# Optimization experiments

Measured on AMD Instinct MI355X. Metric: run time of the kernel, lower is better.

Reference implementation:

```python
import jax, jax.numpy as jnp
import numpy as np

HEADS = 8
DIM_HEAD = 32
DIM = 256
HIDDEN = HEADS * DIM_HEAD  # 256


def setup_inputs() -> dict:
    key = jax.random.key(0)
    ks = jax.random.split(key, 6)
    B, T, C, H, W = 4, 16, DIM, 32, 32
    x = jax.random.normal(ks[0], (B, T, C, H, W), dtype=jnp.float32)
    rel_pos = jax.random.normal(ks[1], (HEADS, T, T), dtype=jnp.float32)
    # 1x1 conv weights == channel-mixing matrices
    w_qkv = jax.random.normal(ks[2], (3 * HIDDEN, C), dtype=jnp.float32) * (C ** -0.5)
    b_qkv = jnp.zeros((3 * HIDDEN,), dtype=jnp.float32)
    w_out = jax.random.normal(ks[3], (C, HIDDEN), dtype=jnp.float32) * (HIDDEN ** -0.5)
    b_out = jnp.zeros((C,), dtype=jnp.float32)
    return {"x": x, "rel_pos": rel_pos, "w_qkv": w_qkv, "b_qkv": b_qkv,
            "w_out": w_out, "b_out": b_out}


def reference(x, rel_pos, w_qkv, b_qkv, w_out, b_out):
    B, T, C, H, W = x.shape
    scale = DIM_HEAD ** -0.5
    # 1x1 conv QKV projection: (B,T,C,H,W) x (3*hidden, C) -> (B,T,H,W,3*hidden)
    qkv = jnp.einsum('btchw,oc->bthwo', x, w_qkv) + b_qkv
    q, k, v = jnp.split(qkv, 3, axis=-1)
    # split heads: (B,T,H,W,heads,dim_head); attention over T per (b,h,w,head)
    q = q.reshape(B, T, H, W, HEADS, DIM_HEAD) * scale
    k = k.reshape(B, T, H, W, HEADS, DIM_HEAD)
    v = v.reshape(B, T, H, W, HEADS, DIM_HEAD)
    # sim: (B,H,W,heads,T,T)
    sim = jnp.einsum('bihwnd,bjhwnd->bhwnij', q, k)
    sim = sim + rel_pos  # (heads,T,T) broadcasts over (B,H,W)
    attn = jax.nn.softmax(sim, axis=-1)
    out = jnp.einsum('bhwnij,bjhwnd->bihwnd', attn, v)  # (B,T,H,W,heads,dh)
    out = out.reshape(B, T, H, W, HIDDEN)
    # 1x1 conv output projection back to C channels
    y = jnp.einsum('bthwe,ce->bthwc', out, w_out) + b_out
    return jnp.transpose(y, (0, 1, 4, 2, 3))  # (B,T,C,H,W)
```

## Files before the change

kernel.cpp:

```cpp
#include <hip/hip_runtime.h>
#include <hip/hip_bf16.h>

typedef __attribute__((ext_vector_type(8))) short bf16x8;
typedef __attribute__((ext_vector_type(4))) float f32x4;
typedef __attribute__((ext_vector_type(16))) float f32x16;

namespace {

constexpr int kT = 16;
constexpr int kC = 256;
constexpr int kHW = 1024;

__device__ __forceinline__ unsigned short f2bf(float f) {
  unsigned int x;
  __builtin_memcpy(&x, &f, 4);
  x += 0x7fff + ((x >> 16) & 1);
  return (unsigned short)(x >> 16);
}
__device__ __forceinline__ unsigned int pack2(float a, float b) {
  return (unsigned int)f2bf(a) | ((unsigned int)f2bf(b) << 16);
}

__global__ __launch_bounds__(256) void prep(const float* __restrict__ x,
                                            const float* __restrict__ wqkv,
                                            const float* __restrict__ wout,
                                            unsigned short* __restrict__ xT,
                                            unsigned short* __restrict__ wAll) {
  __shared__ unsigned short ts[64 * 72];
  const int bx = blockIdx.x;
  const int tid = threadIdx.x;
  if (bx < 4096) {
    const int cc = bx & 3, hc = (bx >> 2) & 15, t = (bx >> 6) & 15, b = bx >> 10;
    const int c0 = cc * 64, hw0 = hc * 64;
    {
      const int ci = tid >> 2, j = tid & 3;
      const float* xrow = x + (((size_t)(b * 16 + t) * 256 + c0 + ci) * 1024) + hw0;
#pragma unroll
      for (int u = 0; u < 4; ++u) {
        const int chunk = j + u * 4;
        const float4 v = *(const float4*)(xrow + chunk * 4);
        const int hwl = chunk * 4;
        ts[(hwl + 0) * 72 + ci] = f2bf(v.x);
        ts[(hwl + 1) * 72 + ci] = f2bf(v.y);
        ts[(hwl + 2) * 72 + ci] = f2bf(v.z);
        ts[(hwl + 3) * 72 + ci] = f2bf(v.w);
      }
    }
    __syncthreads();
    {
      const int hwp = tid >> 2, jp = tid & 3;
      const uint4 a = *(const uint4*)&ts[hwp * 72 + jp * 16];
      const uint4 bq = *(const uint4*)&ts[hwp * 72 + jp * 16 + 8];
      unsigned short* dst =
          xT + ((size_t)((b * 1024 + hw0 + hwp) * 16 + t) * 256) + c0 + jp * 16;
      *(uint4*)dst = a;
      *(uint4*)(dst + 8) = bq;
    }
  } else {
    const int g = bx - 4096;
    const int row_l = tid >> 3;
    const int seg = tid & 7;
    const float* src;
    int srow;
    if (g < 24) { src = wqkv; srow = (g % 3) * 256 + (g / 3) * 32 + row_l; }
    else        { src = wout; srow = (g - 24) * 32 + row_l; }
    const float* s = src + (size_t)srow * 256 + seg * 32;
    unsigned short* d = wAll + ((size_t)(g * 32 + row_l)) * 256 + seg * 32;
#pragma unroll
    for (int u = 0; u < 8; ++u) {
      const float4 v = *(const float4*)(s + u * 4);
      uint2 p;
      p.x = pack2(v.x, v.y);
      p.y = pack2(v.z, v.w);
      *(uint2*)(d + u * 4) = p;
    }
  }
}

constexpr int kWBStride = 264;
constexpr int kWBTile = 32 * kWBStride;
constexpr int kWB = 2 * kWBTile;
constexpr int kSite = 1824;
constexpr int kSmem = kWB + 8 * kSite;
static_assert(kSmem * 2 <= 65536, "LDS budget");

__global__ __launch_bounds__(512, 2) void attn_main(
    const unsigned short* __restrict__ xT,
    const float* __restrict__ rel,
    const unsigned short* __restrict__ wAll,
    const float* __restrict__ bqkv,
    const float* __restrict__ bout,
    float* __restrict__ out) {
  __shared__ __align__(16) unsigned short smem[kSmem];
  const int tid = threadIdx.x;
  const int lane = tid & 63;
  const int wave = tid >> 6;
  const int quad = lane >> 4;
  const int lrow = lane & 15;
  const int half = lane >> 5;
  const int n32 = lane & 31;
  const int b = blockIdx.x >> 6;
  const int hw0 = (blockIdx.x & 63) * 16;
  const int site0 = hw0 + wave * 2;

  bf16x8 ax[16];
  {
    const unsigned short* xs =
        xT + (((size_t)(b * 1024 + site0 + (n32 >> 4))) << 12) + lrow * 256;
#pragma unroll
    for (int ks = 0; ks < 16; ++ks)
      ax[ks] = *(const bf16x8*)(xs + ks * 16 + half * 8);
  }

  unsigned short* qb = smem + kWB + wave * kSite;
  unsigned short* kb = qb + 640;
  unsigned short* vt = qb + 1280;

  const int stageDst = (tid >> 4) * kWBStride + (tid & 15) * 16;
  const int stageSrcOff = (tid >> 4) * 256 + (tid & 15) * 16;

  uint4 pr0, pr1;
  {
    const unsigned short* sp = wAll + stageSrcOff;
    pr0 = *(const uint4*)sp;
    pr1 = *(const uint4*)(sp + 8);
  }

  const f32x4 zero4 = {0.f, 0.f, 0.f, 0.f};
  const float scale = 0.17677669529663687f;
  bf16x8 ao[2][8];

  auto qkv_tile = [&](int g, float bias) -> f32x16 {
    __syncthreads();
    unsigned short* WBc = smem + (g & 1) * kWBTile;
    *(uint4*)(WBc + stageDst) = pr0;
    *(uint4*)(WBc + stageDst + 8) = pr1;
    {
      const unsigned short* sp = wAll + (size_t)(g + 1) * 32 * 256 + stageSrcOff;
      pr0 = *(const uint4*)sp;
      pr1 = *(const uint4*)(sp + 8);
    }
    __syncthreads();
    f32x16 acc;
#pragma unroll
    for (int i = 0; i < 16; ++i) acc[i] = bias;
    const unsigned short* br = WBc + n32 * kWBStride + half * 8;
#pragma unroll
    for (int ks = 0; ks < 16; ++ks) {
      const bf16x8 bf = *(const bf16x8*)(br + ks * 16);
      acc = __builtin_amdgcn_mfma_f32_32x32x16_bf16(ax[ks], bf, acc, 0, 0, 0);
    }
    return acc;
  };

  auto head_body = [&](int h) {
    const f32x16 qacc = qkv_tile(h * 3 + 0, bqkv[h * 32 + n32]);
    const f32x16 kacc = qkv_tile(h * 3 + 1, bqkv[256 + h * 32 + n32]);
    const f32x16 vacc = qkv_tile(h * 3 + 2, bqkv[512 + h * 32 + n32]);
    float rl[4];
#pragma unroll
    for (int r = 0; r < 4; ++r) rl[r] = rel[h * 256 + (quad * 4 + r) * 16 + lrow];

#pragma unroll
    for (int s = 0; s < 2; ++s) {
#pragma unroll
      for (int rr = 0; rr < 8; ++rr) {
        const int t = (rr & 3) + 8 * (rr >> 2) + 4 * half;
        qb[t * 40 + n32] = f2bf(qacc[8 * s + rr]);
        kb[t * 40 + n32] = f2bf(kacc[8 * s + rr]);
      }
#pragma unroll
      for (int rp = 0; rp < 4; ++rp) {
        const int rr = rp * 2;
        const int t = (rr & 3) + 8 * (rr >> 2) + 4 * half;
        *(unsigned int*)&vt[n32 * 16 + t] =
            pack2(vacc[8 * s + rr], vacc[8 * s + rr + 1]);
      }
      const bf16x8 qf = *(const bf16x8*)(qb + lrow * 40 + quad * 8);
      const bf16x8 kf = *(const bf16x8*)(kb + lrow * 40 + quad * 8);
      const f32x4 sim = __builtin_amdgcn_mfma_f32_16x16x32_bf16(qf, kf, zero4, 0, 0, 0);
      float p[4], inv[4];
#pragma unroll
      for (int r = 0; r < 4; ++r) {
        const float v = sim[r] * scale + rl[r];
        float m = v;
        for (int off = 8; off; off >>= 1) m = fmaxf(m, __shfl_xor(m, off));
        const float e = __expf(v - m);
        float sum = e;
        for (int off = 8; off; off >>= 1) sum += __shfl_xor(sum, off);
        p[r] = e;
        inv[r] = 1.0f / sum;
      }
      unsigned short* pb = kb;
#pragma unroll
      for (int r = 0; r < 4; ++r) pb[(quad * 4 + r) * 24 + lrow] = f2bf(p[r]);
      bf16x8 pf, vf0, vf1;
      if (quad < 2) {
        pf = *(const bf16x8*)(pb + lrow * 24 + quad * 8);
        vf0 = *(const bf16x8*)(vt + lrow * 16 + quad * 8);
        vf1 = *(const bf16x8*)(vt + (16 + lrow) * 16 + quad * 8);
      } else {
#pragma unroll
        for (int j = 0; j < 8; ++j) { pf[j] = 0; vf0[j] = 0; vf1[j] = 0; }
      }
      const f32x4 o0 = __builtin_amdgcn_mfma_f32_16x16x32_bf16(pf, vf0, zero4, 0, 0, 0);
      const f32x4 o1 = __builtin_amdgcn_mfma_f32_16x16x32_bf16(pf, vf1, zero4, 0, 0, 0);
#pragma unroll
      for (int r = 0; r < 4; ++r) {
        const int t = quad * 4 + r;
        qb[t * 40 + lrow] = f2bf(o0[r] * inv[r]);
        qb[t * 40 + 16 + lrow] = f2bf(o1[r] * inv[r]);
      }
      ao[s][h] = *(const bf16x8*)(qb + lrow * 40 + quad * 8);
    }
  };

  head_body(0);
  head_body(1);
  head_body(2);
  head_body(3);
  head_body(4);
  head_body(5);
  head_body(6);
  head_body(7);

  __syncthreads();
  float* fbuf = (float*)smem;
  float* ob = out + ((size_t)b << 22);
#pragma unroll 1
  for (int cc = 0; cc < 8; ++cc) {
#pragma unroll
    for (int sub = 0; sub < 2; ++sub) {
      const int c = cc * 32 + sub * 16 + lrow;
      const float bias = bout[c];
      f32x4 y0 = {bias, bias, bias, bias};
      f32x4 y1 = {bias, bias, bias, bias};
#pragma unroll
      for (int ks = 0; ks < 8; ++ks) {
        const bf16x8 wf =
            *(const bf16x8*)(wAll + (size_t)(768 + c) * 256 + ks * 32 + quad * 8);
        y0 = __builtin_amdgcn_mfma_f32_16x16x32_bf16(ao[0][ks], wf, y0, 0, 0, 0);
        y1 = __builtin_amdgcn_mfma_f32_16x16x32_bf16(ao[1][ks], wf, y1, 0, 0, 0);
      }
#pragma unroll
      for (int r = 0; r < 4; ++r) {
        const int t = quad * 4 + r;
        const int L = (t * 32 + sub * 16 + lrow) * 17 + wave * 2;
        fbuf[L] = y0[r];
        fbuf[L + 1] = y1[r];
      }
    }
    __syncthreads();
    {
      const int t = tid >> 5, cl = tid & 31;
      float v[16];
#pragma unroll
      for (int i = 0; i < 16; ++i) v[i] = fbuf[tid * 17 + i];
      float* dst = ob + ((size_t)(t * 256 + cc * 32 + cl)) * 1024 + hw0;
#pragma unroll
      for (int u = 0; u < 4; ++u) {
        float4 q;
        q.x = v[u * 4]; q.y = v[u * 4 + 1]; q.z = v[u * 4 + 2]; q.w = v[u * 4 + 3];
        *(float4*)(dst + u * 4) = q;
      }
    }
    __syncthreads();
  }
}

constexpr int kHWT = 4;
constexpr int kXsTStride = kC * kHWT + 8;
constexpr int kXSize = kT * kXsTStride;
constexpr int kWsOff = kXSize;
constexpr int kWsStride = 264;
constexpr int kWsSize = 32 * kWsStride;
constexpr int kQbOff = kWsOff + kWsSize;
constexpr int kQbWave = 1792;
constexpr int kLdsElems = kQbOff + 4 * kQbWave;

__global__ __launch_bounds__(256, 2) void fused_temporal_attn(
    const float* __restrict__ x, const float* __restrict__ rel,
    const float* __restrict__ wqkv, const float* __restrict__ bqkv,
    const float* __restrict__ wout, const float* __restrict__ bout,
    float* __restrict__ out) {
  __shared__ __align__(16) unsigned short smem[kLdsElems];
  const int tid = threadIdx.x;
  const int lane = tid & 63;
  const int wave = tid >> 6;
  const int quad = lane >> 4;
  const int lrow = lane & 15;
  const int b = blockIdx.x >> 8;
  const int tile = blockIdx.x & 255;
  const int hw0 = tile * kHWT;
  {
    const float* xb = x + (size_t)b * kT * kC * kHW + hw0;
#pragma unroll
    for (int it = 0; it < 16; ++it) {
      int idx = it * 256 + tid;
      int t = idx >> 8, c = idx & 255;
      const float4 v = *(const float4*)(xb + (size_t)(t * kC + c) * kHW);
      uint2 p;
      p.x = pack2(v.x, v.y);
      p.y = pack2(v.z, v.w);
      *(uint2*)&smem[t * kXsTStride + c * kHWT] = p;
    }
  }
  __syncthreads();
  bf16x8 ax[8];
#pragma unroll
  for (int ks = 0; ks < 8; ++ks) {
    bf16x8 f;
#pragma unroll
    for (int j = 0; j < 8; ++j) {
      int c = ks * 32 + quad * 8 + j;
      f[j] = (short)smem[lrow * kXsTStride + c * kHWT + wave];
    }
    ax[ks] = f;
  }
  unsigned short* qb = &smem[kQbOff + wave * kQbWave];
  unsigned short* kbuf = qb + 512;
  unsigned short* vtb = qb + 1024;
  unsigned short* pb = qb + 1536;
  const f32x4 zero4 = {0.f, 0.f, 0.f, 0.f};
  bf16x8 ao[8];
  for (int head = 0; head < 8; ++head) {
    for (int sel = 0; sel < 3; ++sel) {
      __syncthreads();
      {
        const float* wbp = wqkv + (size_t)(sel * 256 + head * 32) * kC;
#pragma unroll
        for (int i = 0; i < 8; ++i) {
          int seg = i * 256 + tid;
          int d = seg >> 6, s = seg & 63;
          const float4 v = *(const float4*)(wbp + d * kC + s * 4);
          uint2 p;
          p.x = pack2(v.x, v.y);
          p.y = pack2(v.z, v.w);
          *(uint2*)&smem[kWsOff + d * kWsStride + s * 4] = p;
        }
      }
      __syncthreads();
      float bias0 = bqkv[sel * 256 + head * 32 + lrow];
      float bias1 = bqkv[sel * 256 + head * 32 + 16 + lrow];
      f32x4 acc0 = {bias0, bias0, bias0, bias0};
      f32x4 acc1 = {bias1, bias1, bias1, bias1};
#pragma unroll
      for (int ks = 0; ks < 8; ++ks) {
        bf16x8 b0 = *(const bf16x8*)&smem[kWsOff + lrow * kWsStride + ks * 32 + quad * 8];
        bf16x8 b1 = *(const bf16x8*)&smem[kWsOff + (16 + lrow) * kWsStride + ks * 32 + quad * 8];
        acc0 = __builtin_amdgcn_mfma_f32_16x16x32_bf16(ax[ks], b0, acc0, 0, 0, 0);
        acc1 = __builtin_amdgcn_mfma_f32_16x16x32_bf16(ax[ks], b1, acc1, 0, 0, 0);
      }
      if (sel < 2) {
        unsigned short* dst = sel ? kbuf : qb;
#pragma unroll
        for (int r = 0; r < 4; ++r) {
          int row = quad * 4 + r;
          dst[row * 32 + lrow] = f2bf(acc0[r]);
          dst[row * 32 + 16 + lrow] = f2bf(acc1[r]);
        }
      } else {
#pragma unroll
        for (int r = 0; r < 4; ++r) {
          int row = quad * 4 + r;
          vtb[lrow * 16 + row] = f2bf(acc0[r]);
          vtb[(16 + lrow) * 16 + row] = f2bf(acc1[r]);
        }
      }
    }
    bf16x8 qf = *(const bf16x8*)&qb[lrow * 32 + quad * 8];
    bf16x8 kf = *(const bf16x8*)&kbuf[lrow * 32 + quad * 8];
    f32x4 sim = __builtin_amdgcn_mfma_f32_16x16x32_bf16(qf, kf, zero4, 0, 0, 0);
    const float scale = 0.17677669529663687f;
    float p[4], rsum[4];
#pragma unroll
    for (int r = 0; r < 4; ++r) {
      int i = quad * 4 + r;
      float v = sim[r] * scale + rel[head * 256 + i * 16 + lrow];
      float m = v;
      for (int off = 8; off; off >>= 1) m = fmaxf(m, __shfl_xor(m, off));
      float e = __expf(v - m);
      float s = e;
      for (int off = 8; off; off >>= 1) s += __shfl_xor(s, off);
      p[r] = e;
      rsum[r] = s;
    }
#pragma unroll
    for (int r = 0; r < 4; ++r) pb[(quad * 4 + r) * 16 + lrow] = f2bf(p[r]);
    bf16x8 pf, vf0, vf1;
    if (quad < 2) {
      pf = *(const bf16x8*)&pb[lrow * 16 + quad * 8];
      vf0 = *(const bf16x8*)&vtb[lrow * 16 + quad * 8];
      vf1 = *(const bf16x8*)&vtb[(16 + lrow) * 16 + quad * 8];
    } else {
#pragma unroll
      for (int j = 0; j < 8; ++j) { pf[j] = 0; vf0[j] = 0; vf1[j] = 0; }
    }
    f32x4 o0 = __builtin_amdgcn_mfma_f32_16x16x32_bf16(pf, vf0, zero4, 0, 0, 0);
    f32x4 o1 = __builtin_amdgcn_mfma_f32_16x16x32_bf16(pf, vf1, zero4, 0, 0, 0);
#pragma unroll
    for (int r = 0; r < 4; ++r) {
      int t = quad * 4 + r;
      float inv = 1.0f / rsum[r];
      qb[t * 32 + lrow] = f2bf(o0[r] * inv);
      qb[t * 32 + 16 + lrow] = f2bf(o1[r] * inv);
    }
    ao[head] = *(const bf16x8*)&qb[lrow * 32 + quad * 8];
  }
  float* ob = out + (size_t)b * kT * kC * kHW + hw0 + wave;
#pragma unroll 1
  for (int nt = 0; nt < 16; ++nt) {
    int c = nt * 16 + lrow;
    float bias = bout[c];
    f32x4 y = {bias, bias, bias, bias};
#pragma unroll
    for (int ks = 0; ks < 8; ++ks) {
      const float4 w0 = *(const float4*)(wout + (size_t)c * kC + ks * 32 + quad * 8);
      const float4 w1 = *(const float4*)(wout + (size_t)c * kC + ks * 32 + quad * 8 + 4);
      bf16x8 wf;
      wf[0] = (short)f2bf(w0.x); wf[1] = (short)f2bf(w0.y);
      wf[2] = (short)f2bf(w0.z); wf[3] = (short)f2bf(w0.w);
      wf[4] = (short)f2bf(w1.x); wf[5] = (short)f2bf(w1.y);
      wf[6] = (short)f2bf(w1.z); wf[7] = (short)f2bf(w1.w);
      y = __builtin_amdgcn_mfma_f32_16x16x32_bf16(ao[ks], wf, y, 0, 0, 0);
    }
#pragma unroll
    for (int r = 0; r < 4; ++r) {
      int t = quad * 4 + r;
      ob[(size_t)(t * kC + c) * kHW] = y[r];
    }
  }
}

}

extern "C" void kernel_launch(void* const* d_in, const int* in_sizes, int n_in,
                              void* d_out, int out_size, void* d_ws, size_t ws_size,
                              hipStream_t stream) {
  const float* x = (const float*)d_in[0];
  const float* rel = (const float*)d_in[1];
  const float* wqkv = (const float*)d_in[2];
  const float* bqkv = (const float*)d_in[3];
  const float* wout = (const float*)d_in[4];
  const float* bout = (const float*)d_in[5];
  float* out = (float*)d_out;
  (void)in_sizes; (void)n_in; (void)out_size;

  constexpr size_t kXTElems = (size_t)4 * 1024 * 16 * 256;
  constexpr size_t kWAllElems = 1024 * 256;
  constexpr size_t kNeed = (kXTElems + kWAllElems) * sizeof(unsigned short);

  if (ws_size >= kNeed) {
    unsigned short* xT = (unsigned short*)d_ws;
    unsigned short* wAll = xT + kXTElems;
    prep<<<4096 + 32, 256, 0, stream>>>(x, wqkv, wout, xT, wAll);
    attn_main<<<256, 512, 0, stream>>>(xT, rel, wAll, bqkv, bout, out);
  } else {
    fused_temporal_attn<<<1024, 256, 0, stream>>>(x, rel, wqkv, bqkv, wout, bout, out);
  }
}
```

Before: 214.8 us.

## Halve attn_main block size to 4 waves, doubling grid with swizzled block mapping

Shrinks each attn_main block from 8 waves covering 16 spatial sites to 4 waves covering 8 sites, launching 512 blocks instead of 256 so more CUs get work and LDS use per block drops. Block IDs are remapped with a swizzle over batch and spatial tiles, the weight-staging copy is widened to 64 bytes per thread, and the qkv biases are preloaded into registers. The cost is that each block re-stages the full weight set for half as many sites, doubling total weight traffic through LDS, and the output stores become shorter 32-byte runs per channel row.

```diff
diff --git a/kernel.cpp b/kernel.cpp
--- a/kernel.cpp
+++ b/kernel.cpp
@@ -81,10 +81,11 @@
 constexpr int kWBTile = 32 * kWBStride;
 constexpr int kWB = 2 * kWBTile;
 constexpr int kSite = 1824;
-constexpr int kSmem = kWB + 8 * kSite;
+constexpr int kSmem = kWB + 4 * kSite;
 static_assert(kSmem * 2 <= 65536, "LDS budget");
-
-__global__ __launch_bounds__(512, 2) void attn_main(
+static_assert(512 * 9 * 4 <= kSmem * 2, "fbuf fits");
+
+__global__ __launch_bounds__(256, 2) void attn_main(
     const unsigned short* __restrict__ xT,
     const float* __restrict__ rel,
     const unsigned short* __restrict__ wAll,
@@ -99,8 +100,10 @@
   const int lrow = lane & 15;
   const int half = lane >> 5;
   const int n32 = lane & 31;
-  const int b = blockIdx.x >> 6;
-  const int hw0 = (blockIdx.x & 63) * 16;
+  const int bid = blockIdx.x;
+  const int vid = (bid & 7) * 64 + (bid >> 3);
+  const int b = vid >> 7;
+  const int hw0 = (vid & 127) * 8;
   const int site0 = hw0 + wave * 2;
 
   bf16x8 ax[16];
@@ -112,18 +115,26 @@
       ax[ks] = *(const bf16x8*)(xs + ks * 16 + half * 8);
   }
 
+  float bq0[8], bk0[8], bv0[8];
+#pragma unroll
+  for (int h = 0; h < 8; ++h) {
+    bq0[h] = bqkv[h * 32 + n32];
+    bk0[h] = bqkv[256 + h * 32 + n32];
+    bv0[h] = bqkv[512 + h * 32 + n32];
+  }
+
   unsigned short* qb = smem + kWB + wave * kSite;
   unsigned short* kb = qb + 640;
   unsigned short* vt = qb + 1280;
 
-  const int stageDst = (tid >> 4) * kWBStride + (tid & 15) * 16;
-  const int stageSrcOff = (tid >> 4) * 256 + (tid & 15) * 16;
-
-  uint4 pr0, pr1;
+  const int stageDst = (tid >> 3) * kWBStride + (tid & 7) * 32;
+  const int stageSrcOff = (tid >> 3) * 256 + (tid & 7) * 32;
+
+  uint4 pr[4];
   {
     const unsigned short* sp = wAll + stageSrcOff;
-    pr0 = *(const uint4*)sp;
-    pr1 = *(const uint4*)(sp + 8);
+#pragma unroll
+    for (int i = 0; i < 4; ++i) pr[i] = *(const uint4*)(sp + i * 8);
   }
 
   const f32x4 zero4 = {0.f, 0.f, 0.f, 0.f};
@@ -133,12 +144,12 @@
   auto qkv_tile = [&](int g, float bias) -> f32x16 {
     __syncthreads();
     unsigned short* WBc = smem + (g & 1) * kWBTile;
-    *(uint4*)(WBc + stageDst) = pr0;
-    *(uint4*)(WBc + stageDst + 8) = pr1;
+#pragma unroll
+    for (int i = 0; i < 4; ++i) *(uint4*)(WBc + stageDst + i * 8) = pr[i];
     {
       const unsigned short* sp = wAll + (size_t)(g + 1) * 32 * 256 + stageSrcOff;
-      pr0 = *(const uint4*)sp;
-      pr1 = *(const uint4*)(sp + 8);
+#pragma unroll
+      for (int i = 0; i < 4; ++i) pr[i] = *(const uint4*)(sp + i * 8);
     }
     __syncthreads();
     f32x16 acc;
@@ -154,9 +165,9 @@
   };
 
   auto head_body = [&](int h) {
-    const f32x16 qacc = qkv_tile(h * 3 + 0, bqkv[h * 32 + n32]);
-    const f32x16 kacc = qkv_tile(h * 3 + 1, bqkv[256 + h * 32 + n32]);
-    const f32x16 vacc = qkv_tile(h * 3 + 2, bqkv[512 + h * 32 + n32]);
+    const f32x16 qacc = qkv_tile(h * 3 + 0, bq0[h]);
+    const f32x16 kacc = qkv_tile(h * 3 + 1, bk0[h]);
+    const f32x16 vacc = qkv_tile(h * 3 + 2, bv0[h]);
     float rl[4];
 #pragma unroll
     for (int r = 0; r < 4; ++r) rl[r] = rel[h * 256 + (quad * 4 + r) * 16 + lrow];
@@ -245,24 +256,25 @@
 #pragma unroll
       for (int r = 0; r < 4; ++r) {
         const int t = quad * 4 + r;
-        const int L = (t * 32 + sub * 16 + lrow) * 17 + wave * 2;
+        const int L = (t * 32 + sub * 16 + lrow) * 9 + wave * 2;
         fbuf[L] = y0[r];
         fbuf[L + 1] = y1[r];
       }
     }
     __syncthreads();
-    {
-      const int t = tid >> 5, cl = tid & 31;
-      float v[16];
-#pragma unroll
-      for (int i = 0; i < 16; ++i) v[i] = fbuf[tid * 17 + i];
+#pragma unroll
+    for (int q2 = 0; q2 < 2; ++q2) {
+      const int L = tid + q2 * 256;
+      const int t = L >> 5, cl = L & 31;
+      float v[8];
+#pragma unroll
+      for (int i = 0; i < 8; ++i) v[i] = fbuf[L * 9 + i];
       float* dst = ob + ((size_t)(t * 256 + cc * 32 + cl)) * 1024 + hw0;
-#pragma unroll
-      for (int u = 0; u < 4; ++u) {
-        float4 q;
-        q.x = v[u * 4]; q.y = v[u * 4 + 1]; q.z = v[u * 4 + 2]; q.w = v[u * 4 + 3];
-        *(float4*)(dst + u * 4) = q;
-      }
+      float4 st0, st1;
+      st0.x = v[0]; st0.y = v[1]; st0.z = v[2]; st0.w = v[3];
+      st1.x = v[4]; st1.y = v[5]; st1.z = v[6]; st1.w = v[7];
+      *(float4*)dst = st0;
+      *(float4*)(dst + 4) = st1;
     }
     __syncthreads();
   }
@@ -454,7 +466,7 @@
     unsigned short* xT = (unsigned short*)d_ws;
     unsigned short* wAll = xT + kXTElems;
     prep<<<4096 + 32, 256, 0, stream>>>(x, wqkv, wout, xT, wAll);
-    attn_main<<<256, 512, 0, stream>>>(xT, rel, wAll, bqkv, bout, out);
+    attn_main<<<512, 256, 0, stream>>>(xT, rel, wAll, bqkv, bout, out);
   } else {
     fused_temporal_attn<<<1024, 256, 0, stream>>>(x, rel, wqkv, bqkv, wout, bout, out);
   }
```

New measurement: 282.6 us. 31.6% more time.

## Use 1024-thread blocks with one site per wave and per-head QKV staging

Applied to the files above, without the earlier changes.

The attention kernel now launches 1024 threads per block, and each of the 16 waves handles one spatial site instead of two. The QKV projection switches from 32x32x16 MFMAs to pairs of 16x16x32 MFMAs. All three q/k/v weight tiles for a head are staged into LDS together, which cuts barriers from three per head to one. The epilogue writes two channel groups per barrier round. Together these aim to raise the number of waves in flight and cut synchronisation, at the cost of more LDS (up to about 128KiB) and one block per CU.

```diff
diff --git a/kernel.cpp b/kernel.cpp
--- a/kernel.cpp
+++ b/kernel.cpp
@@ -3,7 +3,6 @@
 
 typedef __attribute__((ext_vector_type(8))) short bf16x8;
 typedef __attribute__((ext_vector_type(4))) float f32x4;
-typedef __attribute__((ext_vector_type(16))) float f32x16;
 
 namespace {
 
@@ -79,12 +78,13 @@
 
 constexpr int kWBStride = 264;
 constexpr int kWBTile = 32 * kWBStride;
-constexpr int kWB = 2 * kWBTile;
+constexpr int kWG = 3 * kWBTile;
 constexpr int kSite = 1824;
-constexpr int kSmem = kWB + 8 * kSite;
-static_assert(kSmem * 2 <= 65536, "LDS budget");
-
-__global__ __launch_bounds__(512, 2) void attn_main(
+constexpr int kSmem = kWG + 16 * kSite;
+static_assert(kSmem * 2 <= 131072, "LDS within guide-proven 128KiB envelope");
+static_assert(2 * 512 * 17 * 4 <= kSmem * 2, "epilogue fbuf fits");
+
+__global__ __launch_bounds__(1024) void attn_main(
     const unsigned short* __restrict__ xT,
     const float* __restrict__ rel,
     const unsigned short* __restrict__ wAll,
@@ -97,122 +97,129 @@
   const int wave = tid >> 6;
   const int quad = lane >> 4;
   const int lrow = lane & 15;
-  const int half = lane >> 5;
-  const int n32 = lane & 31;
   const int b = blockIdx.x >> 6;
   const int hw0 = (blockIdx.x & 63) * 16;
-  const int site0 = hw0 + wave * 2;
-
-  bf16x8 ax[16];
+  const int site = hw0 + wave;
+
+  bf16x8 ax[8];
   {
     const unsigned short* xs =
-        xT + (((size_t)(b * 1024 + site0 + (n32 >> 4))) << 12) + lrow * 256;
-#pragma unroll
-    for (int ks = 0; ks < 16; ++ks)
-      ax[ks] = *(const bf16x8*)(xs + ks * 16 + half * 8);
-  }
-
-  unsigned short* qb = smem + kWB + wave * kSite;
+        xT + (((size_t)(b * 1024 + site)) << 12) + lrow * 256;
+#pragma unroll
+    for (int ks = 0; ks < 8; ++ks)
+      ax[ks] = *(const bf16x8*)(xs + ks * 32 + quad * 8);
+  }
+
+  unsigned short* qb = smem + kWG + wave * kSite;
   unsigned short* kb = qb + 640;
   unsigned short* vt = qb + 1280;
 
-  const int stageDst = (tid >> 4) * kWBStride + (tid & 15) * 16;
-  const int stageSrcOff = (tid >> 4) * 256 + (tid & 15) * 16;
-
-  uint4 pr0, pr1;
+  const int srow = tid >> 5;
+  const int scol = (tid & 31) * 8;
+  const int stageDst = srow * kWBStride + scol;
+  const int stageSrc = srow * 256 + scol;
+
+  uint4 pr[3];
   {
-    const unsigned short* sp = wAll + stageSrcOff;
-    pr0 = *(const uint4*)sp;
-    pr1 = *(const uint4*)(sp + 8);
+#pragma unroll
+    for (int u = 0; u < 3; ++u)
+      pr[u] = *(const uint4*)(wAll + (size_t)u * 8192 + stageSrc);
   }
 
   const f32x4 zero4 = {0.f, 0.f, 0.f, 0.f};
   const float scale = 0.17677669529663687f;
-  bf16x8 ao[2][8];
-
-  auto qkv_tile = [&](int g, float bias) -> f32x16 {
+  bf16x8 ao[8];
+
+  auto proj = [&](int selIdx, float bias0, float bias1, f32x4& acc0, f32x4& acc1) {
+    const unsigned short* W = smem + selIdx * kWBTile;
+    acc0 = f32x4{bias0, bias0, bias0, bias0};
+    acc1 = f32x4{bias1, bias1, bias1, bias1};
+#pragma unroll
+    for (int ks = 0; ks < 8; ++ks) {
+      const bf16x8 w0 = *(const bf16x8*)(W + lrow * kWBStride + ks * 32 + quad * 8);
+      const bf16x8 w1 = *(const bf16x8*)(W + (16 + lrow) * kWBStride + ks * 32 + quad * 8);
+      acc0 = __builtin_amdgcn_mfma_f32_16x16x32_bf16(ax[ks], w0, acc0, 0, 0, 0);
+      acc1 = __builtin_amdgcn_mfma_f32_16x16x32_bf16(ax[ks], w1, acc1, 0, 0, 0);
+    }
+  };
+
+  auto head_body = [&](int h) {
     __syncthreads();
-    unsigned short* WBc = smem + (g & 1) * kWBTile;
-    *(uint4*)(WBc + stageDst) = pr0;
-    *(uint4*)(WBc + stageDst + 8) = pr1;
+#pragma unroll
+    for (int u = 0; u < 3; ++u)
+      *(uint4*)(smem + u * kWBTile + stageDst) = pr[u];
     {
-      const unsigned short* sp = wAll + (size_t)(g + 1) * 32 * 256 + stageSrcOff;
-      pr0 = *(const uint4*)sp;
-      pr1 = *(const uint4*)(sp + 8);
+      const int gn = 3 * (h + 1);
+#pragma unroll
+      for (int u = 0; u < 3; ++u)
+        pr[u] = *(const uint4*)(wAll + (size_t)(gn + u) * 8192 + stageSrc);
     }
     __syncthreads();
-    f32x16 acc;
-#pragma unroll
-    for (int i = 0; i < 16; ++i) acc[i] = bias;
-    const unsigned short* br = WBc + n32 * kWBStride + half * 8;
-#pragma unroll
-    for (int ks = 0; ks < 16; ++ks) {
-      const bf16x8 bf = *(const bf16x8*)(br + ks * 16);
-      acc = __builtin_amdgcn_mfma_f32_32x32x16_bf16(ax[ks], bf, acc, 0, 0, 0);
-    }
-    return acc;
-  };
-
-  auto head_body = [&](int h) {
-    const f32x16 qacc = qkv_tile(h * 3 + 0, bqkv[h * 32 + n32]);
-    const f32x16 kacc = qkv_tile(h * 3 + 1, bqkv[256 + h * 32 + n32]);
-    const f32x16 vacc = qkv_tile(h * 3 + 2, bqkv[512 + h * 32 + n32]);
+
+    f32x4 a0, a1;
+    proj(0, bqkv[h * 32 + lrow], bqkv[h * 32 + 16 + lrow], a0, a1);
+#pragma unroll
+    for (int r = 0; r < 4; ++r) {
+      const int t = quad * 4 + r;
+      qb[t * 40 + lrow] = f2bf(a0[r]);
+      qb[t * 40 + 16 + lrow] = f2bf(a1[r]);
+    }
+    proj(1, bqkv[256 + h * 32 + lrow], bqkv[256 + h * 32 + 16 + lrow], a0, a1);
+#pragma unroll
+    for (int r = 0; r < 4; ++r) {
+      const int t = quad * 4 + r;
+      kb[t * 40 + lrow] = f2bf(a0[r]);
+      kb[t * 40 + 16 + lrow] = f2bf(a1[r]);
+    }
+    proj(2, bqkv[512 + h * 32 + lrow], bqkv[512 + h * 32 + 16 + lrow], a0, a1);
+#pragma unroll
+    for (int rp = 0; rp < 2; ++rp) {
+      const int r = rp * 2;
+      const int t = quad * 4 + r;
+      *(unsigned int*)&vt[lrow * 16 + t] = pack2(a0[r], a0[r + 1]);
+      *(unsigned int*)&vt[(16 + lrow) * 16 + t] = pack2(a1[r], a1[r + 1]);
+    }
+
     float rl[4];
 #pragma unroll
     for (int r = 0; r < 4; ++r) rl[r] = rel[h * 256 + (quad * 4 + r) * 16 + lrow];
 
-#pragma unroll
-    for (int s = 0; s < 2; ++s) {
-#pragma unroll
-      for (int rr = 0; rr < 8; ++rr) {
-        const int t = (rr & 3) + 8 * (rr >> 2) + 4 * half;
-        qb[t * 40 + n32] = f2bf(qacc[8 * s + rr]);
-        kb[t * 40 + n32] = f2bf(kacc[8 * s + rr]);
-      }
-#pragma unroll
-      for (int rp = 0; rp < 4; ++rp) {
-        const int rr = rp * 2;
-        const int t = (rr & 3) + 8 * (rr >> 2) + 4 * half;
-        *(unsigned int*)&vt[n32 * 16 + t] =
-            pack2(vacc[8 * s + rr], vacc[8 * s + rr + 1]);
-      }
-      const bf16x8 qf = *(const bf16x8*)(qb + lrow * 40 + quad * 8);
-      const bf16x8 kf = *(const bf16x8*)(kb + lrow * 40 + quad * 8);
-      const f32x4 sim = __builtin_amdgcn_mfma_f32_16x16x32_bf16(qf, kf, zero4, 0, 0, 0);
-      float p[4], inv[4];
-#pragma unroll
-      for (int r = 0; r < 4; ++r) {
-        const float v = sim[r] * scale + rl[r];
-        float m = v;
-        for (int off = 8; off; off >>= 1) m = fmaxf(m, __shfl_xor(m, off));
-        const float e = __expf(v - m);
-        float sum = e;
-        for (int off = 8; off; off >>= 1) sum += __shfl_xor(sum, off);
-        p[r] = e;
-        inv[r] = 1.0f / sum;
-      }
-      unsigned short* pb = kb;
-#pragma unroll
-      for (int r = 0; r < 4; ++r) pb[(quad * 4 + r) * 24 + lrow] = f2bf(p[r]);
-      bf16x8 pf, vf0, vf1;
-      if (quad < 2) {
-        pf = *(const bf16x8*)(pb + lrow * 24 + quad * 8);
-        vf0 = *(const bf16x8*)(vt + lrow * 16 + quad * 8);
-        vf1 = *(const bf16x8*)(vt + (16 + lrow) * 16 + quad * 8);
-      } else {
-#pragma unroll
-        for (int j = 0; j < 8; ++j) { pf[j] = 0; vf0[j] = 0; vf1[j] = 0; }
-      }
-      const f32x4 o0 = __builtin_amdgcn_mfma_f32_16x16x32_bf16(pf, vf0, zero4, 0, 0, 0);
-      const f32x4 o1 = __builtin_amdgcn_mfma_f32_16x16x32_bf16(pf, vf1, zero4, 0, 0, 0);
-#pragma unroll
-      for (int r = 0; r < 4; ++r) {
-        const int t = quad * 4 + r;
-        qb[t * 40 + lrow] = f2bf(o0[r] * inv[r]);
-        qb[t * 40 + 16 + lrow] = f2bf(o1[r] * inv[r]);
-      }
-      ao[s][h] = *(const bf16x8*)(qb + lrow * 40 + quad * 8);
-    }
+    const bf16x8 qf = *(const bf16x8*)(qb + lrow * 40 + quad * 8);
+    const bf16x8 kf = *(const bf16x8*)(kb + lrow * 40 + quad * 8);
+    const f32x4 sim = __builtin_amdgcn_mfma_f32_16x16x32_bf16(qf, kf, zero4, 0, 0, 0);
+    float p[4], inv[4];
+#pragma unroll
+    for (int r = 0; r < 4; ++r) {
+      const float v = sim[r] * scale + rl[r];
+      float m = v;
+      for (int off = 8; off; off >>= 1) m = fmaxf(m, __shfl_xor(m, off));
+      const float e = __expf(v - m);
+      float sum = e;
+      for (int off = 8; off; off >>= 1) sum += __shfl_xor(sum, off);
+      p[r] = e;
+      inv[r] = 1.0f / sum;
+    }
+    unsigned short* pb = kb;
+#pragma unroll
+    for (int r = 0; r < 4; ++r) pb[(quad * 4 + r) * 24 + lrow] = f2bf(p[r]);
+    bf16x8 pf, vf0, vf1;
+    if (quad < 2) {
+      pf = *(const bf16x8*)(pb + lrow * 24 + quad * 8);
+      vf0 = *(const bf16x8*)(vt + lrow * 16 + quad * 8);
+      vf1 = *(const bf16x8*)(vt + (16 + lrow) * 16 + quad * 8);
+    } else {
+#pragma unroll
+      for (int j = 0; j < 8; ++j) { pf[j] = 0; vf0[j] = 0; vf1[j] = 0; }
+    }
+    const f32x4 o0 = __builtin_amdgcn_mfma_f32_16x16x32_bf16(pf, vf0, zero4, 0, 0, 0);
+    const f32x4 o1 = __builtin_amdgcn_mfma_f32_16x16x32_bf16(pf, vf1, zero4, 0, 0, 0);
+#pragma unroll
+    for (int r = 0; r < 4; ++r) {
+      const int t = quad * 4 + r;
+      qb[t * 40 + lrow] = f2bf(o0[r] * inv[r]);
+      qb[t * 40 + 16 + lrow] = f2bf(o1[r] * inv[r]);
+    }
+    ao[h] = *(const bf16x8*)(qb + lrow * 40 + quad * 8);
   };
 
   head_body(0);
@@ -228,35 +235,36 @@
   float* fbuf = (float*)smem;
   float* ob = out + ((size_t)b << 22);
 #pragma unroll 1
-  for (int cc = 0; cc < 8; ++cc) {
-#pragma unroll
-    for (int sub = 0; sub < 2; ++sub) {
-      const int c = cc * 32 + sub * 16 + lrow;
-      const float bias = bout[c];
-      f32x4 y0 = {bias, bias, bias, bias};
-      f32x4 y1 = {bias, bias, bias, bias};
-#pragma unroll
-      for (int ks = 0; ks < 8; ++ks) {
-        const bf16x8 wf =
-            *(const bf16x8*)(wAll + (size_t)(768 + c) * 256 + ks * 32 + quad * 8);
-        y0 = __builtin_amdgcn_mfma_f32_16x16x32_bf16(ao[0][ks], wf, y0, 0, 0, 0);
-        y1 = __builtin_amdgcn_mfma_f32_16x16x32_bf16(ao[1][ks], wf, y1, 0, 0, 0);
-      }
-#pragma unroll
-      for (int r = 0; r < 4; ++r) {
-        const int t = quad * 4 + r;
-        const int L = (t * 32 + sub * 16 + lrow) * 17 + wave * 2;
-        fbuf[L] = y0[r];
-        fbuf[L + 1] = y1[r];
+  for (int cp = 0; cp < 4; ++cp) {
+#pragma unroll
+    for (int g = 0; g < 2; ++g) {
+      const int cc = cp * 2 + g;
+#pragma unroll
+      for (int sub = 0; sub < 2; ++sub) {
+        const int c = cc * 32 + sub * 16 + lrow;
+        const float bias = bout[c];
+        f32x4 y = {bias, bias, bias, bias};
+#pragma unroll
+        for (int ks = 0; ks < 8; ++ks) {
+          const bf16x8 wf =
+              *(const bf16x8*)(wAll + (size_t)(768 + c) * 256 + ks * 32 + quad * 8);
+          y = __builtin_amdgcn_mfma_f32_16x16x32_bf16(ao[ks], wf, y, 0, 0, 0);
+        }
+#pragma unroll
+        for (int r = 0; r < 4; ++r) {
+          const int t = quad * 4 + r;
+          fbuf[g * 8704 + (t * 32 + sub * 16 + lrow) * 17 + wave] = y[r];
+        }
       }
     }
     __syncthreads();
     {
-      const int t = tid >> 5, cl = tid & 31;
+      const int g2 = tid >> 9, L = tid & 511;
+      const int t = L >> 5, cl = L & 31;
       float v[16];
 #pragma unroll
-      for (int i = 0; i < 16; ++i) v[i] = fbuf[tid * 17 + i];
-      float* dst = ob + ((size_t)(t * 256 + cc * 32 + cl)) * 1024 + hw0;
+      for (int i = 0; i < 16; ++i) v[i] = fbuf[g2 * 8704 + L * 17 + i];
+      float* dst = ob + ((size_t)(t * 256 + (cp * 2 + g2) * 32 + cl)) * 1024 + hw0;
 #pragma unroll
       for (int u = 0; u < 4; ++u) {
         float4 q;
@@ -454,7 +462,7 @@
     unsigned short* xT = (unsigned short*)d_ws;
     unsigned short* wAll = xT + kXTElems;
     prep<<<4096 + 32, 256, 0, stream>>>(x, wqkv, wout, xT, wAll);
-    attn_main<<<256, 512, 0, stream>>>(xT, rel, wAll, bqkv, bout, out);
+    attn_main<<<256, 1024, 0, stream>>>(xT, rel, wAll, bqkv, bout, out);
   } else {
     fused_temporal_attn<<<1024, 256, 0, stream>>>(x, rel, wqkv, bqkv, wout, bout, out);
   }
```

Result: slower. 254.8 us (+18.7%).

## Fuse x transpose and weight bf16 conversion into main attention kernel

Applied to the files above, without the earlier changes.

Removes the separate prep kernel that transposed x into a bf16 workspace and converted the weights. The main kernel now loads fp32 x panels straight from global memory, converts and transposes them through LDS, and converts the fp32 QKV and output weights to bf16 on the fly. This drops one launch and a full write and read of the bf16 copy of x. The cost is more conversion work and fp32 weight traffic repeated in every block, with only 256 blocks doing the strided x reads. The unused fallback kernel is deleted.

```diff
diff --git a/kernel.cpp b/kernel.cpp
--- a/kernel.cpp
+++ b/kernel.cpp
@@ -6,10 +6,6 @@
 typedef __attribute__((ext_vector_type(16))) float f32x16;
 
 namespace {
-
-constexpr int kT = 16;
-constexpr int kC = 256;
-constexpr int kHW = 1024;
 
 __device__ __forceinline__ unsigned short f2bf(float f) {
   unsigned int x;
@@ -21,74 +17,22 @@
   return (unsigned int)f2bf(a) | ((unsigned int)f2bf(b) << 16);
 }
 
-__global__ __launch_bounds__(256) void prep(const float* __restrict__ x,
-                                            const float* __restrict__ wqkv,
-                                            const float* __restrict__ wout,
-                                            unsigned short* __restrict__ xT,
-                                            unsigned short* __restrict__ wAll) {
-  __shared__ unsigned short ts[64 * 72];
-  const int bx = blockIdx.x;
-  const int tid = threadIdx.x;
-  if (bx < 4096) {
-    const int cc = bx & 3, hc = (bx >> 2) & 15, t = (bx >> 6) & 15, b = bx >> 10;
-    const int c0 = cc * 64, hw0 = hc * 64;
-    {
-      const int ci = tid >> 2, j = tid & 3;
-      const float* xrow = x + (((size_t)(b * 16 + t) * 256 + c0 + ci) * 1024) + hw0;
-#pragma unroll
-      for (int u = 0; u < 4; ++u) {
-        const int chunk = j + u * 4;
-        const float4 v = *(const float4*)(xrow + chunk * 4);
-        const int hwl = chunk * 4;
-        ts[(hwl + 0) * 72 + ci] = f2bf(v.x);
-        ts[(hwl + 1) * 72 + ci] = f2bf(v.y);
-        ts[(hwl + 2) * 72 + ci] = f2bf(v.z);
-        ts[(hwl + 3) * 72 + ci] = f2bf(v.w);
-      }
-    }
-    __syncthreads();
-    {
-      const int hwp = tid >> 2, jp = tid & 3;
-      const uint4 a = *(const uint4*)&ts[hwp * 72 + jp * 16];
-      const uint4 bq = *(const uint4*)&ts[hwp * 72 + jp * 16 + 8];
-      unsigned short* dst =
-          xT + ((size_t)((b * 1024 + hw0 + hwp) * 16 + t) * 256) + c0 + jp * 16;
-      *(uint4*)dst = a;
-      *(uint4*)(dst + 8) = bq;
-    }
-  } else {
-    const int g = bx - 4096;
-    const int row_l = tid >> 3;
-    const int seg = tid & 7;
-    const float* src;
-    int srow;
-    if (g < 24) { src = wqkv; srow = (g % 3) * 256 + (g / 3) * 32 + row_l; }
-    else        { src = wout; srow = (g - 24) * 32 + row_l; }
-    const float* s = src + (size_t)srow * 256 + seg * 32;
-    unsigned short* d = wAll + ((size_t)(g * 32 + row_l)) * 256 + seg * 32;
-#pragma unroll
-    for (int u = 0; u < 8; ++u) {
-      const float4 v = *(const float4*)(s + u * 4);
-      uint2 p;
-      p.x = pack2(v.x, v.y);
-      p.y = pack2(v.z, v.w);
-      *(uint2*)(d + u * 4) = p;
-    }
-  }
-}
-
 constexpr int kWBStride = 264;
 constexpr int kWBTile = 32 * kWBStride;
 constexpr int kWB = 2 * kWBTile;
 constexpr int kSite = 1824;
 constexpr int kSmem = kWB + 8 * kSite;
+constexpr int kPanelStride = 72;
 static_assert(kSmem * 2 <= 65536, "LDS budget");
-
-__global__ __launch_bounds__(512, 2) void attn_main(
-    const unsigned short* __restrict__ xT,
+static_assert(16 * 16 * kPanelStride <= kSmem, "x panel fits");
+static_assert(512 * 17 * 4 <= kSmem * 2, "fbuf fits");
+
+__global__ __launch_bounds__(512, 2) void attn_fused(
+    const float* __restrict__ x,
     const float* __restrict__ rel,
-    const unsigned short* __restrict__ wAll,
+    const float* __restrict__ wqkv,
     const float* __restrict__ bqkv,
+    const float* __restrict__ wout,
     const float* __restrict__ bout,
     float* __restrict__ out) {
   __shared__ __align__(16) unsigned short smem[kSmem];
@@ -101,31 +45,51 @@
   const int n32 = lane & 31;
   const int b = blockIdx.x >> 6;
   const int hw0 = (blockIdx.x & 63) * 16;
-  const int site0 = hw0 + wave * 2;
+
+  const int wrow = tid >> 4;
+  const int wcol = (tid & 15) * 16;
+  float4 pw[4];
+  {
+    const float* sp = wqkv + (size_t)wrow * 256 + wcol;
+#pragma unroll
+    for (int u = 0; u < 4; ++u) pw[u] = *(const float4*)(sp + u * 4);
+  }
 
   bf16x8 ax[16];
   {
-    const unsigned short* xs =
-        xT + (((size_t)(b * 1024 + site0 + (n32 >> 4))) << 12) + lrow * 256;
-#pragma unroll
-    for (int ks = 0; ks < 16; ++ks)
-      ax[ks] = *(const bf16x8*)(xs + ks * 16 + half * 8);
+    unsigned short* panel = smem;
+    const int sloc = wave * 2 + (n32 >> 4);
+#pragma unroll
+    for (int cc4 = 0; cc4 < 4; ++cc4) {
+      const int c0 = cc4 * 64;
+      __syncthreads();
+#pragma unroll
+      for (int u = 0; u < 8; ++u) {
+        const int idx = u * 512 + tid;
+        const int row = idx >> 2;
+        const int q = idx & 3;
+        const int t = row >> 6;
+        const int cl = row & 63;
+        const float4 v = *(const float4*)(
+            x + (((size_t)(b * 16 + t) * 256 + c0 + cl) << 10) + hw0 + q * 4);
+        unsigned short* pr = panel + (t * 16 + q * 4) * kPanelStride + cl;
+        pr[0] = f2bf(v.x);
+        pr[kPanelStride] = f2bf(v.y);
+        pr[2 * kPanelStride] = f2bf(v.z);
+        pr[3 * kPanelStride] = f2bf(v.w);
+      }
+      __syncthreads();
+#pragma unroll
+      for (int kk = 0; kk < 4; ++kk)
+        ax[cc4 * 4 + kk] = *(const bf16x8*)(
+            panel + (lrow * 16 + sloc) * kPanelStride + kk * 16 + half * 8);
+    }
   }
 
   unsigned short* qb = smem + kWB + wave * kSite;
   unsigned short* kb = qb + 640;
   unsigned short* vt = qb + 1280;
 
-  const int stageDst = (tid >> 4) * kWBStride + (tid & 15) * 16;
-  const int stageSrcOff = (tid >> 4) * 256 + (tid & 15) * 16;
-
-  uint4 pr0, pr1;
-  {
-    const unsigned short* sp = wAll + stageSrcOff;
-    pr0 = *(const uint4*)sp;
-    pr1 = *(const uint4*)(sp + 8);
-  }
-
   const f32x4 zero4 = {0.f, 0.f, 0.f, 0.f};
   const float scale = 0.17677669529663687f;
   bf16x8 ao[2][8];
@@ -133,12 +97,26 @@
   auto qkv_tile = [&](int g, float bias) -> f32x16 {
     __syncthreads();
     unsigned short* WBc = smem + (g & 1) * kWBTile;
-    *(uint4*)(WBc + stageDst) = pr0;
-    *(uint4*)(WBc + stageDst + 8) = pr1;
     {
-      const unsigned short* sp = wAll + (size_t)(g + 1) * 32 * 256 + stageSrcOff;
-      pr0 = *(const uint4*)sp;
-      pr1 = *(const uint4*)(sp + 8);
+      unsigned short* dst = WBc + wrow * kWBStride + wcol;
+      uint4 a, bq;
+      a.x = pack2(pw[0].x, pw[0].y);
+      a.y = pack2(pw[0].z, pw[0].w);
+      a.z = pack2(pw[1].x, pw[1].y);
+      a.w = pack2(pw[1].z, pw[1].w);
+      bq.x = pack2(pw[2].x, pw[2].y);
+      bq.y = pack2(pw[2].z, pw[2].w);
+      bq.z = pack2(pw[3].x, pw[3].y);
+      bq.w = pack2(pw[3].z, pw[3].w);
+      *(uint4*)dst = a;
+      *(uint4*)(dst + 8) = bq;
+    }
+    {
+      const int gn = g + 1;
+      const int rowbase = (gn % 3) * 256 + (gn / 3) * 32;
+      const float* sp = wqkv + (size_t)(rowbase + wrow) * 256 + wcol;
+#pragma unroll
+      for (int u = 0; u < 4; ++u) pw[u] = *(const float4*)(sp + u * 4);
     }
     __syncthreads();
     f32x16 acc;
@@ -237,8 +215,13 @@
       f32x4 y1 = {bias, bias, bias, bias};
 #pragma unroll
       for (int ks = 0; ks < 8; ++ks) {
-        const bf16x8 wf =
-            *(const bf16x8*)(wAll + (size_t)(768 + c) * 256 + ks * 32 + quad * 8);
+        const float4 w0 = *(const float4*)(wout + (size_t)c * 256 + ks * 32 + quad * 8);
+        const float4 w1 = *(const float4*)(wout + (size_t)c * 256 + ks * 32 + quad * 8 + 4);
+        bf16x8 wf;
+        wf[0] = (short)f2bf(w0.x); wf[1] = (short)f2bf(w0.y);
+        wf[2] = (short)f2bf(w0.z); wf[3] = (short)f2bf(w0.w);
+        wf[4] = (short)f2bf(w1.x); wf[5] = (short)f2bf(w1.y);
+        wf[6] = (short)f2bf(w1.z); wf[7] = (short)f2bf(w1.w);
         y0 = __builtin_amdgcn_mfma_f32_16x16x32_bf16(ao[0][ks], wf, y0, 0, 0, 0);
         y1 = __builtin_amdgcn_mfma_f32_16x16x32_bf16(ao[1][ks], wf, y1, 0, 0, 0);
       }
@@ -265,170 +248,6 @@
       }
     }
     __syncthreads();
-  }
-}
-
-constexpr int kHWT = 4;
-constexpr int kXsTStride = kC * kHWT + 8;
-constexpr int kXSize = kT * kXsTStride;
-constexpr int kWsOff = kXSize;
-constexpr int kWsStride = 264;
-constexpr int kWsSize = 32 * kWsStride;
-constexpr int kQbOff = kWsOff + kWsSize;
-constexpr int kQbWave = 1792;
-constexpr int kLdsElems = kQbOff + 4 * kQbWave;
-
-__global__ __launch_bounds__(256, 2) void fused_temporal_attn(
-    const float* __restrict__ x, const float* __restrict__ rel,
-    const float* __restrict__ wqkv, const float* __restrict__ bqkv,
-    const float* __restrict__ wout, const float* __restrict__ bout,
-    float* __restrict__ out) {
-  __shared__ __align__(16) unsigned short smem[kLdsElems];
-  const int tid = threadIdx.x;
-  const int lane = tid & 63;
-  const int wave = tid >> 6;
-  const int quad = lane >> 4;
-  const int lrow = lane & 15;
-  const int b = blockIdx.x >> 8;
-  const int tile = blockIdx.x & 255;
-  const int hw0 = tile * kHWT;
-  {
-    const float* xb = x + (size_t)b * kT * kC * kHW + hw0;
-#pragma unroll
-    for (int it = 0; it < 16; ++it) {
-      int idx = it * 256 + tid;
-      int t = idx >> 8, c = idx & 255;
-      const float4 v = *(const float4*)(xb + (size_t)(t * kC + c) * kHW);
-      uint2 p;
-      p.x = pack2(v.x, v.y);
-      p.y = pack2(v.z, v.w);
-      *(uint2*)&smem[t * kXsTStride + c * kHWT] = p;
-    }
-  }
-  __syncthreads();
-  bf16x8 ax[8];
-#pragma unroll
-  for (int ks = 0; ks < 8; ++ks) {
-    bf16x8 f;
-#pragma unroll
-    for (int j = 0; j < 8; ++j) {
-      int c = ks * 32 + quad * 8 + j;
-      f[j] = (short)smem[lrow * kXsTStride + c * kHWT + wave];
-    }
-    ax[ks] = f;
-  }
-  unsigned short* qb = &smem[kQbOff + wave * kQbWave];
-  unsigned short* kbuf = qb + 512;
-  unsigned short* vtb = qb + 1024;
-  unsigned short* pb = qb + 1536;
-  const f32x4 zero4 = {0.f, 0.f, 0.f, 0.f};
-  bf16x8 ao[8];
-  for (int head = 0; head < 8; ++head) {
-    for (int sel = 0; sel < 3; ++sel) {
-      __syncthreads();
-      {
-        const float* wbp = wqkv + (size_t)(sel * 256 + head * 32) * kC;
-#pragma unroll
-        for (int i = 0; i < 8; ++i) {
-          int seg = i * 256 + tid;
-          int d = seg >> 6, s = seg & 63;
-          const float4 v = *(const float4*)(wbp + d * kC + s * 4);
-          uint2 p;
-          p.x = pack2(v.x, v.y);
-          p.y = pack2(v.z, v.w);
-          *(uint2*)&smem[kWsOff + d * kWsStride + s * 4] = p;
-        }
-      }
-      __syncthreads();
-      float bias0 = bqkv[sel * 256 + head * 32 + lrow];
-      float bias1 = bqkv[sel * 256 + head * 32 + 16 + lrow];
-      f32x4 acc0 = {bias0, bias0, bias0, bias0};
-      f32x4 acc1 = {bias1, bias1, bias1, bias1};
-#pragma unroll
-      for (int ks = 0; ks < 8; ++ks) {
-        bf16x8 b0 = *(const bf16x8*)&smem[kWsOff + lrow * kWsStride + ks * 32 + quad * 8];
-        bf16x8 b1 = *(const bf16x8*)&smem[kWsOff + (16 + lrow) * kWsStride + ks * 32 + quad * 8];
-        acc0 = __builtin_amdgcn_mfma_f32_16x16x32_bf16(ax[ks], b0, acc0, 0, 0, 0);
-        acc1 = __builtin_amdgcn_mfma_f32_16x16x32_bf16(ax[ks], b1, acc1, 0, 0, 0);
-      }
-      if (sel < 2) {
-        unsigned short* dst = sel ? kbuf : qb;
-#pragma unroll
-        for (int r = 0; r < 4; ++r) {
-          int row = quad * 4 + r;
-          dst[row * 32 + lrow] = f2bf(acc0[r]);
-          dst[row * 32 + 16 + lrow] = f2bf(acc1[r]);
-        }
-      } else {
-#pragma unroll
-        for (int r = 0; r < 4; ++r) {
-          int row = quad * 4 + r;
-          vtb[lrow * 16 + row] = f2bf(acc0[r]);
-          vtb[(16 + lrow) * 16 + row] = f2bf(acc1[r]);
-        }
-      }
-    }
-    bf16x8 qf = *(const bf16x8*)&qb[lrow * 32 + quad * 8];
-    bf16x8 kf = *(const bf16x8*)&kbuf[lrow * 32 + quad * 8];
-    f32x4 sim = __builtin_amdgcn_mfma_f32_16x16x32_bf16(qf, kf, zero4, 0, 0, 0);
-    const float scale = 0.17677669529663687f;
-    float p[4], rsum[4];
-#pragma unroll
-    for (int r = 0; r < 4; ++r) {
-      int i = quad * 4 + r;
-      float v = sim[r] * scale + rel[head * 256 + i * 16 + lrow];
-      float m = v;
-      for (int off = 8; off; off >>= 1) m = fmaxf(m, __shfl_xor(m, off));
-      float e = __expf(v - m);
-      float s = e;
-      for (int off = 8; off; off >>= 1) s += __shfl_xor(s, off);
-      p[r] = e;
-      rsum[r] = s;
-    }
-#pragma unroll
-    for (int r = 0; r < 4; ++r) pb[(quad * 4 + r) * 16 + lrow] = f2bf(p[r]);
-    bf16x8 pf, vf0, vf1;
-    if (quad < 2) {
-      pf = *(const bf16x8*)&pb[lrow * 16 + quad * 8];
-      vf0 = *(const bf16x8*)&vtb[lrow * 16 + quad * 8];
-      vf1 = *(const bf16x8*)&vtb[(16 + lrow) * 16 + quad * 8];
-    } else {
-#pragma unroll
-      for (int j = 0; j < 8; ++j) { pf[j] = 0; vf0[j] = 0; vf1[j] = 0; }
-    }
-    f32x4 o0 = __builtin_amdgcn_mfma_f32_16x16x32_bf16(pf, vf0, zero4, 0, 0, 0);
-    f32x4 o1 = __builtin_amdgcn_mfma_f32_16x16x32_bf16(pf, vf1, zero4, 0, 0, 0);
-#pragma unroll
-    for (int r = 0; r < 4; ++r) {
-      int t = quad * 4 + r;
-      float inv = 1.0f / rsum[r];
-      qb[t * 32 + lrow] = f2bf(o0[r] * inv);
-      qb[t * 32 + 16 + lrow] = f2bf(o1[r] * inv);
-    }
-    ao[head] = *(const bf16x8*)&qb[lrow * 32 + quad * 8];
-  }
-  float* ob = out + (size_t)b * kT * kC * kHW + hw0 + wave;
-#pragma unroll 1
-  for (int nt = 0; nt < 16; ++nt) {
-    int c = nt * 16 + lrow;
-    float bias = bout[c];
-    f32x4 y = {bias, bias, bias, bias};
-#pragma unroll
-    for (int ks = 0; ks < 8; ++ks) {
-      const float4 w0 = *(const float4*)(wout + (size_t)c * kC + ks * 32 + quad * 8);
-      const float4 w1 = *(const float4*)(wout + (size_t)c * kC + ks * 32 + quad * 8 + 4);
-      bf16x8 wf;
-      wf[0] = (short)f2bf(w0.x); wf[1] = (short)f2bf(w0.y);
-      wf[2] = (short)f2bf(w0.z); wf[3] = (short)f2bf(w0.w);
-      wf[4] = (short)f2bf(w1.x); wf[5] = (short)f2bf(w1.y);
-      wf[6] = (short)f2bf(w1.z); wf[7] = (short)f2bf(w1.w);
-      y = __builtin_amdgcn_mfma_f32_16x16x32_bf16(ao[ks], wf, y, 0, 0, 0);
-    }
-#pragma unroll
-    for (int r = 0; r < 4; ++r) {
-      int t = quad * 4 + r;
-      ob[(size_t)(t * kC + c) * kHW] = y[r];
-    }
   }
 }
 
@@ -444,18 +263,7 @@
   const float* wout = (const float*)d_in[4];
   const float* bout = (const float*)d_in[5];
   float* out = (float*)d_out;
-  (void)in_sizes; (void)n_in; (void)out_size;
-
-  constexpr size_t kXTElems = (size_t)4 * 1024 * 16 * 256;
-  constexpr size_t kWAllElems = 1024 * 256;
-  constexpr size_t kNeed = (kXTElems + kWAllElems) * sizeof(unsigned short);
-
-  if (ws_size >= kNeed) {
-    unsigned short* xT = (unsigned short*)d_ws;
-    unsigned short* wAll = xT + kXTElems;
-    prep<<<4096 + 32, 256, 0, stream>>>(x, wqkv, wout, xT, wAll);
-    attn_main<<<256, 512, 0, stream>>>(xT, rel, wAll, bqkv, bout, out);
-  } else {
-    fused_temporal_attn<<<1024, 256, 0, stream>>>(x, rel, wqkv, bqkv, wout, bout, out);
-  }
-}
+  (void)in_sizes; (void)n_in; (void)out_size; (void)d_ws; (void)ws_size;
+
+  attn_fused<<<256, 512, 0, stream>>>(x, rel, wqkv, bqkv, wout, bout, out);
+}
```

Result: slower. 245.5 us (+14.3%).
